# Optimization experiments

Measured on AMD Instinct MI355X. Metric: run time of the kernel, lower is better.

## Reference

```python
import jax, jax.numpy as jnp
import numpy as np

B, P, T = 4096, 16, 8
IN_DIM, OUT_DIM, K = 128, 128, 2
N_TABLE = 100000


def setup_inputs() -> dict:
    key = jax.random.key(0)
    ks = jax.random.split(key, 8)
    return {
        "path_input": jax.random.randint(ks[0], (B, P, T), 0, N_TABLE, dtype=jnp.int32),
        "path_num": P,
        "timestamp": T,
        "path_type": jax.random.randint(ks[1], (T,), 0, 4, dtype=jnp.int32),
        "user_emb": jax.random.normal(ks[2], (N_TABLE, IN_DIM), jnp.float32),
        "item_emb": jax.random.normal(ks[3], (N_TABLE, IN_DIM), jnp.float32),
        "ca_emb": jax.random.normal(ks[4], (N_TABLE, IN_DIM), jnp.float32),
        "ci_emb": jax.random.normal(ks[5], (N_TABLE, IN_DIM), jnp.float32),
        "conv_w": jax.random.normal(ks[6], (OUT_DIM, IN_DIM, K), jnp.float32) * 0.05,
        "conv_b": jax.random.normal(ks[7], (OUT_DIM,), jnp.float32) * 0.05,
    }


def reference(path_input, path_num, timestamp, path_type,
              user_emb, item_emb, ca_emb, ci_emb, conv_w, conv_b):
    b, p, t = path_input.shape
    # [4, N, D] stacked tables; per-position table selection via path_type
    tables = jnp.stack([user_emb, item_emb, ca_emb, ci_emb])
    # emb: [B, P, T, D]  (advanced indexing: path_type broadcasts over B, P)
    emb = tables[path_type[None, None, :], path_input]
    # conv1d over time: [B*P, D, T] -> [B*P, out, T-K+1]
    x = emb.reshape(b * p, t, -1).transpose(0, 2, 1)
    y = jax.lax.conv_general_dilated(
        x, conv_w, window_strides=(1,), padding='VALID',
        dimension_numbers=('NCH', 'OIH', 'NCH')) + conv_b[None, :, None]
    # max-pool over time, then over paths (dropout is identity in eval)
    y = y.max(axis=-1).reshape(b, p, -1)  # [B, P, out]
    return y.max(axis=1)  # [B, out]
```

## Files before the change

### kernel.cpp

```cpp
#include <hip/hip_runtime.h>

#define NB   4096
#define NBLK 512
#define NJ   8

typedef __attribute__((ext_vector_type(4))) float f32x4;
typedef __attribute__((ext_vector_type(8))) short short8;
typedef __attribute__((ext_vector_type(4))) int   int4v;
typedef __attribute__((ext_vector_type(2))) int   int2v;

union Frag { int4v i; short8 s; };

__device__ __forceinline__ unsigned short f2bf(float f) {
  unsigned int u = __float_as_uint(f);
  u = (u + 0x7FFFu + ((u >> 16) & 1u)) >> 16;
  return (unsigned short)u;
}

__device__ __forceinline__ int cvtpk(float lo, float hi) {
  int r;
  asm("v_cvt_pk_bf16_f32 %0, %1, %2" : "=v"(r) : "v"(lo), "v"(hi));
  return r;
}

__global__ __launch_bounds__(512)
void wconv_kernel(const float* __restrict__ conv_w, unsigned short* __restrict__ ws)
{
  int flat = blockIdx.x * 512 + threadIdx.x;
  int lane = flat & 63;
  int ng   = (flat >> 6) & 7;
  int ker  = (flat >> 9) & 1;
  int kk   = flat >> 10;
  int col  = ng * 16 + (lane & 15);
  int k0   = kk * 32 + (lane >> 4) * 8;
  short8 s;
#pragma unroll
  for (int j = 0; j < 8; ++j)
    s[j] = (short)f2bf(conv_w[col * 256 + (k0 + j) * 2 + ker]);
  *(short8*)(ws + (size_t)flat * 8) = s;
}

#define A0_OFF  0
#define A1_OFF  34816
#define RED_OFF 69632
#define IDX_OFF 70656
#define PTR_OFF 74752
#define LDS_BYTES 74816
#define A_STRIDE 272

__global__ __launch_bounds__(512, 2)
void path_emb_kernel(const int* __restrict__ path_input,
                     const int* __restrict__ path_type,
                     const float* __restrict__ t0, const float* __restrict__ t1,
                     const float* __restrict__ t2, const float* __restrict__ t3,
                     const unsigned short* __restrict__ wfrag,
                     const float* __restrict__ conv_b,
                     float* __restrict__ out)
{
  __shared__ __align__(16) char lds[LDS_BYTES];
  const int blk  = blockIdx.x;
  const int tid  = threadIdx.x;
  const int wid  = tid >> 6;
  const int lane = tid & 63;
  const int lrow = lane & 15;
  const int lk   = lane >> 4;
  const int R = wid & 1;
  const int C = wid >> 1;

  if (tid < NJ * 128 / 4)
    ((int4v*)(lds + IDX_OFF))[tid] =
        ((const int4v*)(path_input + (size_t)blk * NJ * 128))[tid];
  if (tid < 8) {
    int ty = path_type[tid];
    const float* tb = (ty == 0) ? t0 : (ty == 1) ? t1 : (ty == 2) ? t2 : t3;
    ((const float**)(lds + PTR_OFF))[tid] = tb;
  }
  float cb = (tid < 128) ? conv_b[tid] : 0.0f;

  Frag wreg[4][2][2];
#pragma unroll
  for (int kk = 0; kk < 4; ++kk)
#pragma unroll
    for (int ker = 0; ker < 2; ++ker)
#pragma unroll
      for (int n = 0; n < 2; ++n) {
        int f = (kk * 2 + ker) * 8 + C * 2 + n;
        wreg[kk][ker][n].i = *(const int4v*)(wfrag + (size_t)f * 512 + lane * 8);
      }
  __syncthreads();

  const int grow = tid >> 2;
  const int gq   = tid & 3;

  auto ISSUE = [&](int j, f32x4 (&ld)[8]) {
    int idx = ((const int*)(lds + IDX_OFF))[j * 128 + grow];
    const float* tb = ((const float* const*)(lds + PTR_OFF))[grow & 7];
    const float* g  = tb + (size_t)idx * 128 + gq * 4;
#pragma unroll
    for (int i = 0; i < 8; ++i) ld[i] = *(const f32x4*)(g + i * 16);
  };
  auto WRITE = [&](int bufoff, const f32x4 (&ld)[8]) {
    char* dst = lds + bufoff + grow * A_STRIDE + gq * 8;
#pragma unroll
    for (int i = 0; i < 8; ++i) {
      int2v w;
      w[0] = cvtpk(ld[i][0], ld[i][1]);
      w[1] = cvtpk(ld[i][2], ld[i][3]);
      *(int2v*)(dst + i * 32) = w;
    }
  };

  float* red = (float*)(lds + RED_OFF);
  const int arow0 = R * 64 + lrow;

  auto COMPUTE = [&](int bufc) {
    f32x4 accA[4][2] = {};
    f32x4 accB[4][2] = {};
    const char* Ab = lds + bufc;
#pragma unroll
    for (int kk = 0; kk < 4; ++kk) {
      Frag a[4];
#pragma unroll
      for (int m = 0; m < 4; ++m)
        a[m].i = *(const int4v*)(Ab + (arow0 + m * 16) * A_STRIDE + kk * 64 + lk * 16);
#pragma unroll
      for (int m = 0; m < 4; ++m)
#pragma unroll
        for (int n = 0; n < 2; ++n) {
          accA[m][n] = __builtin_amdgcn_mfma_f32_16x16x32_bf16(
              a[m].s, wreg[kk][0][n].s, accA[m][n], 0, 0, 0);
          accB[m][n] = __builtin_amdgcn_mfma_f32_16x16x32_bf16(
              a[m].s, wreg[kk][1][n].s, accB[m][n], 0, 0, 0);
        }
    }
    float vmax[2] = {-1e30f, -1e30f};
#pragma unroll
    for (int m = 0; m < 4; ++m)
#pragma unroll
      for (int n = 0; n < 2; ++n) {
        float up = __shfl_down(accB[m][n][0], 16);
#pragma unroll
        for (int r = 0; r < 4; ++r) {
          int rloc = lk * 4 + r;
          if ((rloc & 7) == 7) continue;
          float y2 = (r < 3) ? accB[m][n][r + 1] : up;
          vmax[n] = fmaxf(vmax[n], accA[m][n][r] + y2);
        }
      }
#pragma unroll
    for (int n = 0; n < 2; ++n) {
      float v = vmax[n];
      v = fmaxf(v, __shfl_xor(v, 16));
      v = fmaxf(v, __shfl_xor(v, 32));
      vmax[n] = v;
    }
    if (lane < 16) {
#pragma unroll
      for (int n = 0; n < 2; ++n)
        red[R * 128 + C * 32 + n * 16 + lane] = vmax[n];
    }
  };

  auto BAR = [&]() {
    asm volatile("s_waitcnt lgkmcnt(0)" ::: "memory");
    __builtin_amdgcn_sched_barrier(0);
    __builtin_amdgcn_s_barrier();
    __builtin_amdgcn_sched_barrier(0);
  };

  f32x4 ld[8];
  ISSUE(0, ld);
  WRITE(A0_OFF, ld);
  BAR();

#pragma unroll 1
  for (int j = 0; j < NJ; ++j) {
    const int bufc = (j & 1) ? A1_OFF : A0_OFF;
    const int bufn = (j & 1) ? A0_OFF : A1_OFF;
    const bool pf  = (j + 1 < NJ);

    if (pf) ISSUE(j + 1, ld);
    __builtin_amdgcn_sched_barrier(0);

    COMPUTE(bufc);
    BAR();

    if (pf) WRITE(bufn, ld);

    if (tid < 128)
      out[(size_t)(blk * NJ + j) * 128 + tid] =
          fmaxf(red[tid], red[128 + tid]) + cb;

    BAR();
  }
}

extern "C" void kernel_launch(void* const* d_in, const int* in_sizes, int n_in,
                              void* d_out, int out_size, void* d_ws, size_t ws_size,
                              hipStream_t stream) {
  const int*   path_input = (const int*)d_in[0];
  const int*   path_type  = (const int*)d_in[3];
  const float* user_emb   = (const float*)d_in[4];
  const float* item_emb   = (const float*)d_in[5];
  const float* ca_emb     = (const float*)d_in[6];
  const float* ci_emb     = (const float*)d_in[7];
  const float* conv_w     = (const float*)d_in[8];
  const float* conv_b     = (const float*)d_in[9];
  float* out = (float*)d_out;
  unsigned short* wfrag = (unsigned short*)d_ws;

  wconv_kernel<<<dim3(8), dim3(512), 0, stream>>>(conv_w, wfrag);
  path_emb_kernel<<<dim3(NBLK), dim3(512), 0, stream>>>(
      path_input, path_type, user_emb, item_emb, ca_emb, ci_emb,
      wfrag, conv_b, out);
}
```

Baseline: 52.80 us.

## Deepen gather prefetch to three register buffers and fuse conv taps into single accumulator

Halves the grid so each block handles 16 batch rows, and replaces the double-buffered LDS tile with a single LDS tile plus three register-resident prefetch buffers, keeping three gathers in flight. The two conv taps now accumulate into one accumulator by reading the next time row from LDS, removing the second accumulator set and the cross-lane shuffle. Indices and table pointers are read directly from global memory instead of being staged in LDS. The aim is more memory-latency hiding and lower LDS use, at the cost of higher register pressure from the three buffers and the fully unrolled loop, and fewer blocks in the grid.

Measured after the change: 53.89 us. 2.1% more time.

```diff
diff --git a/kernel.cpp b/kernel.cpp
--- a/kernel.cpp
+++ b/kernel.cpp
@@ -1,8 +1,8 @@
 #include <hip/hip_runtime.h>
 
 #define NB   4096
-#define NBLK 512
-#define NJ   8
+#define NBLK 256
+#define NJ   16
 
 typedef __attribute__((ext_vector_type(4))) float f32x4;
 typedef __attribute__((ext_vector_type(8))) short short8;
@@ -40,15 +40,11 @@
   *(short8*)(ws + (size_t)flat * 8) = s;
 }
 
-#define A0_OFF  0
-#define A1_OFF  34816
-#define RED_OFF 69632
-#define IDX_OFF 70656
-#define PTR_OFF 74752
-#define LDS_BYTES 74816
+#define RED_OFF 35088
+#define LDS_BYTES 36112
 #define A_STRIDE 272
 
-__global__ __launch_bounds__(512, 2)
+__global__ __launch_bounds__(512)
 void path_emb_kernel(const int* __restrict__ path_input,
                      const int* __restrict__ path_type,
                      const float* __restrict__ t0, const float* __restrict__ t1,
@@ -67,15 +63,13 @@
   const int R = wid & 1;
   const int C = wid >> 1;
 
-  if (tid < NJ * 128 / 4)
-    ((int4v*)(lds + IDX_OFF))[tid] =
-        ((const int4v*)(path_input + (size_t)blk * NJ * 128))[tid];
-  if (tid < 8) {
-    int ty = path_type[tid];
-    const float* tb = (ty == 0) ? t0 : (ty == 1) ? t1 : (ty == 2) ? t2 : t3;
-    ((const float**)(lds + PTR_OFF))[tid] = tb;
-  }
+  const int* idxg = path_input + (size_t)blk * NJ * 128;
   float cb = (tid < 128) ? conv_b[tid] : 0.0f;
+
+  const int grow = tid >> 2;
+  const int gq   = tid & 3;
+  const int ty   = path_type[grow & 7];
+  const float* tb = (ty == 0) ? t0 : (ty == 1) ? t1 : (ty == 2) ? t2 : t3;
 
   Frag wreg[4][2][2];
 #pragma unroll
@@ -87,20 +81,15 @@
         int f = (kk * 2 + ker) * 8 + C * 2 + n;
         wreg[kk][ker][n].i = *(const int4v*)(wfrag + (size_t)f * 512 + lane * 8);
       }
-  __syncthreads();
-
-  const int grow = tid >> 2;
-  const int gq   = tid & 3;
 
   auto ISSUE = [&](int j, f32x4 (&ld)[8]) {
-    int idx = ((const int*)(lds + IDX_OFF))[j * 128 + grow];
-    const float* tb = ((const float* const*)(lds + PTR_OFF))[grow & 7];
-    const float* g  = tb + (size_t)idx * 128 + gq * 4;
+    int idx = idxg[j * 128 + grow];
+    const float* g = tb + (size_t)idx * 128 + gq * 4;
 #pragma unroll
     for (int i = 0; i < 8; ++i) ld[i] = *(const f32x4*)(g + i * 16);
   };
-  auto WRITE = [&](int bufoff, const f32x4 (&ld)[8]) {
-    char* dst = lds + bufoff + grow * A_STRIDE + gq * 8;
+  auto WRITE = [&](const f32x4 (&ld)[8]) {
+    char* dst = lds + grow * A_STRIDE + gq * 8;
 #pragma unroll
     for (int i = 0; i < 8; ++i) {
       int2v w;
@@ -113,40 +102,38 @@
   float* red = (float*)(lds + RED_OFF);
   const int arow0 = R * 64 + lrow;
 
-  auto COMPUTE = [&](int bufc) {
-    f32x4 accA[4][2] = {};
-    f32x4 accB[4][2] = {};
-    const char* Ab = lds + bufc;
+  auto COMPUTE = [&]() {
+    f32x4 acc[4][2] = {};
 #pragma unroll
     for (int kk = 0; kk < 4; ++kk) {
-      Frag a[4];
+      Frag alo[4], ahi[4];
+#pragma unroll
+      for (int m = 0; m < 4; ++m) {
+        const char* p = lds + (arow0 + m * 16) * A_STRIDE + kk * 64 + lk * 16;
+        alo[m].i = *(const int4v*)(p);
+        ahi[m].i = *(const int4v*)(p + A_STRIDE);
+      }
 #pragma unroll
       for (int m = 0; m < 4; ++m)
-        a[m].i = *(const int4v*)(Ab + (arow0 + m * 16) * A_STRIDE + kk * 64 + lk * 16);
-#pragma unroll
-      for (int m = 0; m < 4; ++m)
 #pragma unroll
         for (int n = 0; n < 2; ++n) {
-          accA[m][n] = __builtin_amdgcn_mfma_f32_16x16x32_bf16(
-              a[m].s, wreg[kk][0][n].s, accA[m][n], 0, 0, 0);
-          accB[m][n] = __builtin_amdgcn_mfma_f32_16x16x32_bf16(
-              a[m].s, wreg[kk][1][n].s, accB[m][n], 0, 0, 0);
+          acc[m][n] = __builtin_amdgcn_mfma_f32_16x16x32_bf16(
+              alo[m].s, wreg[kk][0][n].s, acc[m][n], 0, 0, 0);
+          acc[m][n] = __builtin_amdgcn_mfma_f32_16x16x32_bf16(
+              ahi[m].s, wreg[kk][1][n].s, acc[m][n], 0, 0, 0);
         }
     }
     float vmax[2] = {-1e30f, -1e30f};
 #pragma unroll
     for (int m = 0; m < 4; ++m)
 #pragma unroll
-      for (int n = 0; n < 2; ++n) {
-        float up = __shfl_down(accB[m][n][0], 16);
+      for (int n = 0; n < 2; ++n)
 #pragma unroll
         for (int r = 0; r < 4; ++r) {
           int rloc = lk * 4 + r;
           if ((rloc & 7) == 7) continue;
-          float y2 = (r < 3) ? accB[m][n][r + 1] : up;
-          vmax[n] = fmaxf(vmax[n], accA[m][n][r] + y2);
+          vmax[n] = fmaxf(vmax[n], acc[m][n][r]);
         }
-      }
 #pragma unroll
     for (int n = 0; n < 2; ++n) {
       float v = vmax[n];
@@ -168,29 +155,34 @@
     __builtin_amdgcn_sched_barrier(0);
   };
 
-  f32x4 ld[8];
-  ISSUE(0, ld);
-  WRITE(A0_OFF, ld);
+  f32x4 lA[8], lB[8], lC[8];
+  ISSUE(0, lA);
+  ISSUE(1, lB);
+  ISSUE(2, lC);
+  WRITE(lA);
   BAR();
 
-#pragma unroll 1
+#pragma unroll
   for (int j = 0; j < NJ; ++j) {
-    const int bufc = (j & 1) ? A1_OFF : A0_OFF;
-    const int bufn = (j & 1) ? A0_OFF : A1_OFF;
-    const bool pf  = (j + 1 < NJ);
-
-    if (pf) ISSUE(j + 1, ld);
+    if (j + 3 < NJ) {
+      if (j % 3 == 0)      ISSUE(j + 3, lA);
+      else if (j % 3 == 1) ISSUE(j + 3, lB);
+      else                 ISSUE(j + 3, lC);
+    }
     __builtin_amdgcn_sched_barrier(0);
 
-    COMPUTE(bufc);
+    COMPUTE();
     BAR();
-
-    if (pf) WRITE(bufn, ld);
 
     if (tid < 128)
       out[(size_t)(blk * NJ + j) * 128 + tid] =
           fmaxf(red[tid], red[128 + tid]) + cb;
 
+    if (j + 1 < NJ) {
+      if ((j + 1) % 3 == 0)      WRITE(lA);
+      else if ((j + 1) % 3 == 1) WRITE(lB);
+      else                       WRITE(lC);
+    }
     BAR();
   }
 }
```
